# Kernel tuning notes

Hardware: AMD Instinct MI355X
Metric: run time of the kernel (lower is better)

## Reference

```python
import jax, jax.numpy as jnp
import numpy as np

N = 100000
E = 1600000
F = 128
COMP_RATIO = 4
K = max(1, N // COMP_RATIO)


def mean_agg(x, src, tgt, n):
    # mean over in-neighbors: h_i = mean_{(j->i) in edges} x_j
    s = jax.ops.segment_sum(x[src], tgt, num_segments=n)          # [N, F]
    cnt = jax.ops.segment_sum(jnp.ones(src.shape[0], x.dtype), tgt, num_segments=n)
    return s / jnp.maximum(cnt, 1.0)[:, None]


def setup_inputs() -> dict:
    key = jax.random.key(0)
    ks = jax.random.split(key, 10)
    sc = 1.0 / np.sqrt(F)
    return {
        "x": jax.random.normal(ks[0], (N, F), jnp.float32),
        "src": jax.random.randint(ks[1], (E,), 0, N, jnp.int32),
        "tgt": jax.random.randint(ks[2], (E,), 0, N, jnp.int32),
        "W_self": jax.random.normal(ks[3], (F, F), jnp.float32) * sc,
        "W_neigh": jax.random.normal(ks[4], (F, F), jnp.float32) * sc,
        "b_pack": jnp.zeros((F,), jnp.float32),
        "w_score": jax.random.normal(ks[5], (F, 1), jnp.float32) * sc,
        "b_score": jnp.zeros((1,), jnp.float32),
        "W_u1": jax.random.normal(ks[6], (F, F), jnp.float32) * sc,
        "b_u1": jnp.zeros((F,), jnp.float32),
        "W_u2": jax.random.normal(ks[7], (F, F), jnp.float32) * sc,
        "b_u2": jnp.zeros((F,), jnp.float32),
    }


def reference(x, src, tgt, W_self, W_neigh, b_pack, w_score, b_score,
              W_u1, b_u1, W_u2, b_u2):
    # ---- compress ----
    # SAGEConv (mean aggregator): fc_self(x) + fc_neigh(mean_neigh(x)) + bias
    h = x @ W_self + mean_agg(x, src, tgt, N) @ W_neigh + b_pack  # [N, F]
    # scorer: Linear(F,1) + Sigmoid
    score = jax.nn.sigmoid(h @ w_score + b_score)[:, 0]           # [N]
    # pool: topk scores, gate selected features by their score
    sel_scores, idx = jax.lax.top_k(score, K)                     # [K], [K]
    new_val = h[idx] * sel_scores[:, None]                        # [K, F]
    # ---- decompress ----
    z = jnp.zeros((N, F), x.dtype).at[idx].set(new_val)
    # diffusion layer 1 (SageConvExt update_func='diffuse'):
    # propagate neighbor mean, keep the received (seed) features fixed
    d = mean_agg(z, src, tgt, N) @ W_u1 + b_u1
    d = d.at[idx].set(z[idx])
    d = jax.nn.relu(d)
    # diffusion layer 2
    out = mean_agg(d, src, tgt, N) @ W_u2 + b_u2
    out = out.at[idx].set(d[idx])
    return out
```

## Files before the change

### kernel.cpp

```cpp
#include <hip/hip_runtime.h>

#define NN 100000
#define NE 1600000
#define FF 128
#define KK 25000
#define NB ((NN + 255) / 256)
#define BM 64
#define BK 32
#define GEMM_GRID ((NN + BM - 1) / BM)

#define BKT_SHIFT 11
#define NPBK (1 << BKT_SHIFT)
#define NBKT2 ((NN + NPBK - 1) >> BKT_SHIFT)
#define NBLKA 512
#define CHUNKA ((NE + NBLKA - 1) / NBLKA)

__device__ __forceinline__ unsigned short f2b(float f) {
  unsigned u = __float_as_uint(f);
  u += 0x7FFFu + ((u >> 16) & 1u);
  return (unsigned short)(u >> 16);
}
__device__ __forceinline__ unsigned pack2(float lo, float hi) {
  return (unsigned)f2b(lo) | ((unsigned)f2b(hi) << 16);
}

__device__ __forceinline__ unsigned long long topk_key(float s, unsigned i) {
  return (((unsigned long long)__float_as_uint(s)) << 32) |
         (unsigned long long)(0xFFFFFFFFu - i);
}

__global__ __launch_bounds__(256) void k_histA(const int* __restrict__ tgt,
                                               int* __restrict__ histg) {
  __shared__ int h[NBKT2];
  for (int i = threadIdx.x; i < NBKT2; i += 256) h[i] = 0;
  __syncthreads();
  int b = blockIdx.x;
  int e0 = b * CHUNKA, e1 = min(e0 + CHUNKA, NE);
  for (int e = e0 + threadIdx.x; e < e1; e += 256)
    atomicAdd(&h[tgt[e] >> BKT_SHIFT], 1);
  __syncthreads();
  for (int i = threadIdx.x; i < NBKT2; i += 256) histg[i * NBLKA + b] = h[i];
}

__global__ __launch_bounds__(1024) void k_scanA(int* __restrict__ histg,
                                                int* __restrict__ bbase) {
  const int M = NBKT2 * NBLKA;
  const int C = (M + 1023) / 1024;
  __shared__ int part[1024];
  __shared__ int tmp[1024];
  int t = threadIdx.x;
  int i0 = t * C;
  int iend = min(i0 + C, M);
  int s = 0;
  for (int i = i0; i < iend; ++i) s += histg[i];
  part[t] = s;
  __syncthreads();
  int* A = part;
  int* B = tmp;
  for (int off = 1; off < 1024; off <<= 1) {
    int v = A[t] + (t >= off ? A[t - off] : 0);
    B[t] = v;
    __syncthreads();
    int* sw = A; A = B; B = sw;
  }
  int run = (t > 0) ? A[t - 1] : 0;
  for (int i = i0; i < iend; ++i) {
    int v = histg[i];
    histg[i] = run;
    run += v;
  }
  __syncthreads();
  if (t < NBKT2) bbase[t] = histg[t * NBLKA];
  if (t == 0) bbase[NBKT2] = NE;
}

__global__ __launch_bounds__(256) void k_scatterA(const int* __restrict__ src,
                                                  const int* __restrict__ tgt,
                                                  const int* __restrict__ histg,
                                                  int* __restrict__ pairs) {
  __shared__ int cur[NBKT2];
  int b = blockIdx.x;
  for (int i = threadIdx.x; i < NBKT2; i += 256) cur[i] = histg[i * NBLKA + b];
  __syncthreads();
  int e0 = b * CHUNKA, e1 = min(e0 + CHUNKA, NE);
  for (int e = e0 + threadIdx.x; e < e1; e += 256) {
    int t = tgt[e];
    int p = atomicAdd(&cur[t >> BKT_SHIFT], 1);
    pairs[p] = (src[e] << BKT_SHIFT) | (t & (NPBK - 1));
  }
}

__global__ __launch_bounds__(1024) void k_bucketB(const int* __restrict__ pairs,
                                                  const int* __restrict__ bbase,
                                                  int* __restrict__ offsets,
                                                  int* __restrict__ csr) {
  __shared__ int cnt[NPBK];
  __shared__ int part[1024];
  __shared__ int tmp[1024];
  int b = blockIdx.x;
  int t = threadIdx.x;
  int lo = b << BKT_SHIFT;
  int nloc = min(NPBK, NN - lo);
  int base = bbase[b];
  int cntE = bbase[b + 1] - base;
  cnt[t] = 0;
  cnt[t + 1024] = 0;
  __syncthreads();
  for (int p = t; p < cntE; p += 1024)
    atomicAdd(&cnt[pairs[base + p] & (NPBK - 1)], 1);
  __syncthreads();
  int a0 = cnt[2 * t];
  int a1 = cnt[2 * t + 1];
  part[t] = a0 + a1;
  __syncthreads();
  int* A = part;
  int* B = tmp;
  for (int off = 1; off < 1024; off <<= 1) {
    int v = A[t] + (t >= off ? A[t - off] : 0);
    B[t] = v;
    __syncthreads();
    int* sw = A; A = B; B = sw;
  }
  int o0 = (t > 0) ? A[t - 1] : 0;
  int o1 = o0 + a0;
  if (2 * t < nloc) offsets[lo + 2 * t] = base + o0;
  if (2 * t + 1 < nloc) offsets[lo + 2 * t + 1] = base + o1;
  __syncthreads();
  cnt[2 * t] = o0;
  cnt[2 * t + 1] = o1;
  __syncthreads();
  for (int p = t; p < cntE; p += 1024) {
    int v = pairs[base + p];
    int l = v & (NPBK - 1);
    int pos = atomicAdd(&cnt[l], 1);
    csr[base + pos] = v >> BKT_SHIFT;
  }
  if (b == NBKT2 - 1 && t == 0) offsets[NN] = NE;
}

__global__ __launch_bounds__(256) void k_agg(const float* __restrict__ vals,
                                             const int* __restrict__ csr,
                                             const int* __restrict__ offsets,
                                             float* __restrict__ outv) {
  int w = threadIdx.x >> 6;
  int lane = threadIdx.x & 63;
  int half = lane >> 5;
  int li = lane & 31;
  int node = blockIdx.x * 4 + w;
  if (node >= NN) return;
  int beg = offsets[node];
  int end = offsets[node + 1];
  int deg = end - beg;
  float a0 = 0.f, a1 = 0.f, a2 = 0.f, a3 = 0.f;
  int e = beg;
  int e8 = beg + (deg & ~7);
  for (; e < e8; e += 8) {
    float4 v[4];
#pragma unroll
    for (int q = 0; q < 4; ++q) {
      int j = csr[e + 2 * q + half];
      v[q] = *reinterpret_cast<const float4*>(&vals[(size_t)j * FF + li * 4]);
    }
#pragma unroll
    for (int q = 0; q < 4; ++q) {
      a0 += v[q].x; a1 += v[q].y; a2 += v[q].z; a3 += v[q].w;
    }
  }
  for (; e + 2 <= end; e += 2) {
    int j = csr[e + half];
    float4 v = *reinterpret_cast<const float4*>(&vals[(size_t)j * FF + li * 4]);
    a0 += v.x; a1 += v.y; a2 += v.z; a3 += v.w;
  }
  if (e < end && half == 0) {
    int j = csr[e];
    float4 v = *reinterpret_cast<const float4*>(&vals[(size_t)j * FF + li * 4]);
    a0 += v.x; a1 += v.y; a2 += v.z; a3 += v.w;
  }
  a0 += __shfl_xor(a0, 32, 64);
  a1 += __shfl_xor(a1, 32, 64);
  a2 += __shfl_xor(a2, 32, 64);
  a3 += __shfl_xor(a3, 32, 64);
  if (half == 0) {
    float inv = 1.0f / (float)(deg > 0 ? deg : 1);
    *reinterpret_cast<float4*>(&outv[(size_t)node * FF + li * 4]) =
        make_float4(a0 * inv, a1 * inv, a2 * inv, a3 * inv);
  }
}

template <bool GATED>
__global__ __launch_bounds__(256) void k_agg_bf(const unsigned* __restrict__ vals,
                                                const int* __restrict__ csr,
                                                const int* __restrict__ offsets,
                                                const float* __restrict__ sel,
                                                unsigned* __restrict__ outv) {
  int w = threadIdx.x >> 6;
  int lane = threadIdx.x & 63;
  int qt = lane >> 4;
  int li = lane & 15;
  int node = blockIdx.x * 4 + w;
  if (node >= NN) return;
  int beg = offsets[node];
  int end = offsets[node + 1];
  int deg = end - beg;
  float a0 = 0.f, a1 = 0.f, a2 = 0.f, a3 = 0.f;
  float a4 = 0.f, a5 = 0.f, a6 = 0.f, a7 = 0.f;
  int e = beg;
  int e8 = beg + (deg & ~7);
  for (; e < e8; e += 8) {
    uint4 u[2];
#pragma unroll
    for (int q = 0; q < 2; ++q) {
      int j = csr[e + 4 * q + qt];
      u[q] = (!GATED || sel[j] != 0.f)
                 ? *reinterpret_cast<const uint4*>(&vals[(size_t)j * (FF / 2) + li * 4])
                 : make_uint4(0u, 0u, 0u, 0u);
    }
#pragma unroll
    for (int q = 0; q < 2; ++q) {
      a0 += __uint_as_float(u[q].x << 16);
      a1 += __uint_as_float(u[q].x & 0xFFFF0000u);
      a2 += __uint_as_float(u[q].y << 16);
      a3 += __uint_as_float(u[q].y & 0xFFFF0000u);
      a4 += __uint_as_float(u[q].z << 16);
      a5 += __uint_as_float(u[q].z & 0xFFFF0000u);
      a6 += __uint_as_float(u[q].w << 16);
      a7 += __uint_as_float(u[q].w & 0xFFFF0000u);
    }
  }
  for (; e + 4 <= end; e += 4) {
    int j = csr[e + qt];
    uint4 u = (!GATED || sel[j] != 0.f)
                  ? *reinterpret_cast<const uint4*>(&vals[(size_t)j * (FF / 2) + li * 4])
                  : make_uint4(0u, 0u, 0u, 0u);
    a0 += __uint_as_float(u.x << 16);
    a1 += __uint_as_float(u.x & 0xFFFF0000u);
    a2 += __uint_as_float(u.y << 16);
    a3 += __uint_as_float(u.y & 0xFFFF0000u);
    a4 += __uint_as_float(u.z << 16);
    a5 += __uint_as_float(u.z & 0xFFFF0000u);
    a6 += __uint_as_float(u.w << 16);
    a7 += __uint_as_float(u.w & 0xFFFF0000u);
  }
  int r = end - e;
  if (qt < r) {
    int j = csr[e + qt];
    uint4 u = (!GATED || sel[j] != 0.f)
                  ? *reinterpret_cast<const uint4*>(&vals[(size_t)j * (FF / 2) + li * 4])
                  : make_uint4(0u, 0u, 0u, 0u);
    a0 += __uint_as_float(u.x << 16);
    a1 += __uint_as_float(u.x & 0xFFFF0000u);
    a2 += __uint_as_float(u.y << 16);
    a3 += __uint_as_float(u.y & 0xFFFF0000u);
    a4 += __uint_as_float(u.z << 16);
    a5 += __uint_as_float(u.z & 0xFFFF0000u);
    a6 += __uint_as_float(u.w << 16);
    a7 += __uint_as_float(u.w & 0xFFFF0000u);
  }
  a0 += __shfl_xor(a0, 16, 64); a0 += __shfl_xor(a0, 32, 64);
  a1 += __shfl_xor(a1, 16, 64); a1 += __shfl_xor(a1, 32, 64);
  a2 += __shfl_xor(a2, 16, 64); a2 += __shfl_xor(a2, 32, 64);
  a3 += __shfl_xor(a3, 16, 64); a3 += __shfl_xor(a3, 32, 64);
  a4 += __shfl_xor(a4, 16, 64); a4 += __shfl_xor(a4, 32, 64);
  a5 += __shfl_xor(a5, 16, 64); a5 += __shfl_xor(a5, 32, 64);
  a6 += __shfl_xor(a6, 16, 64); a6 += __shfl_xor(a6, 32, 64);
  a7 += __shfl_xor(a7, 16, 64); a7 += __shfl_xor(a7, 32, 64);
  if (qt == 0) {
    float inv = 1.0f / (float)(deg > 0 ? deg : 1);
    uint4 o;
    o.x = pack2(a0 * inv, a1 * inv);
    o.y = pack2(a2 * inv, a3 * inv);
    o.z = pack2(a4 * inv, a5 * inv);
    o.w = pack2(a6 * inv, a7 * inv);
    *reinterpret_cast<uint4*>(&outv[(size_t)node * (FF / 2) + li * 4]) = o;
  }
}

template <int EPI, bool DUAL, bool ABF16>
__global__ __launch_bounds__(256) void k_gemm4(const void* __restrict__ Araw,
                                               const float* __restrict__ W,
                                               const float* __restrict__ A2,
                                               const float* __restrict__ W2,
                                               const float* __restrict__ bias,
                                               const float* __restrict__ aux,
                                               const float* __restrict__ score,
                                               const float* __restrict__ sel,
                                               float* __restrict__ outv,
                                               unsigned* __restrict__ obf,
                                               const float* __restrict__ wsc,
                                               const float* __restrict__ bsc,
                                               float* __restrict__ score_out) {
  __shared__ float As[BK][BM + 4];
  __shared__ float Ws[BK][FF];
  const int tid = threadIdx.x;
  const int tx = tid & 15;
  const int ty = tid >> 4;
  const int m0 = blockIdx.x * BM;

  float acc[4][8];
#pragma unroll
  for (int r = 0; r < 4; ++r)
#pragma unroll
    for (int j = 0; j < 8; ++j) acc[r][j] = 0.f;

  const int NPASS = DUAL ? 2 : 1;
  for (int pass = 0; pass < NPASS; ++pass) {
    const float* Wp = (pass == 0) ? W : W2;
    for (int kt = 0; kt < FF; kt += BK) {
      __syncthreads();
      if (pass == 0 && ABF16) {
        const unsigned* Ab = (const unsigned*)Araw;
#pragma unroll
        for (int t = 0; t < 4; ++t) {
          int i = tid + t * 256;
          int row = i >> 4;
          int cu = i & 15;
          int gr = m0 + row;
          unsigned u = (gr < NN) ? Ab[(size_t)gr * (FF / 2) + (kt >> 1) + cu] : 0u;
          As[cu * 2 + 0][row] = __uint_as_float(u << 16);
          As[cu * 2 + 1][row] = __uint_as_float(u & 0xFFFF0000u);
        }
      } else {
        const float* Ag = (pass == 0) ? (const float*)Araw : A2;
#pragma unroll
        for (int t = 0; t < 2; ++t) {
          int i = tid + t * 256;
          int row = i >> 3;
          int c8 = i & 7;
          int gr = m0 + row;
          float4 v = make_float4(0.f, 0.f, 0.f, 0.f);
          if (gr < NN) v = *(const float4*)&Ag[(size_t)gr * FF + kt + c8 * 4];
          As[c8 * 4 + 0][row] = v.x;
          As[c8 * 4 + 1][row] = v.y;
          As[c8 * 4 + 2][row] = v.z;
          As[c8 * 4 + 3][row] = v.w;
        }
      }
#pragma unroll
      for (int t = 0; t < 4; ++t) {
        int i = tid + t * 256;
        int kr = i >> 5;
        int c4 = i & 31;
        *(float4*)&Ws[kr][c4 * 4] =
            *(const float4*)&Wp[(size_t)(kt + kr) * FF + c4 * 4];
      }
      __syncthreads();
#pragma unroll
      for (int k = 0; k < BK; ++k) {
        float4 a = *(const float4*)&As[k][ty * 4];
        float4 w0 = *(const float4*)&Ws[k][tx * 4];
        float4 w1 = *(const float4*)&Ws[k][tx * 4 + 64];
        float av[4] = {a.x, a.y, a.z, a.w};
        float wv[8] = {w0.x, w0.y, w0.z, w0.w, w1.x, w1.y, w1.z, w1.w};
#pragma unroll
        for (int r = 0; r < 4; ++r)
#pragma unroll
          for (int j = 0; j < 8; ++j) acc[r][j] = fmaf(av[r], wv[j], acc[r][j]);
      }
    }
  }

  float4 b0 = *(const float4*)&bias[tx * 4];
  float4 b1 = *(const float4*)&bias[tx * 4 + 64];
  float bs[8] = {b0.x, b0.y, b0.z, b0.w, b1.x, b1.y, b1.z, b1.w};

  if constexpr (EPI == 0) {
    __shared__ float sp[BM][17];
    float4 s0 = *(const float4*)&wsc[tx * 4];
    float4 s1 = *(const float4*)&wsc[tx * 4 + 64];
    float sv[8] = {s0.x, s0.y, s0.z, s0.w, s1.x, s1.y, s1.z, s1.w};
#pragma unroll
    for (int r = 0; r < 4; ++r) {
      int gi = m0 + ty * 4 + r;
      if (gi >= NN) continue;
      size_t base = (size_t)gi * FF;
      float v[8];
      float p = 0.f;
#pragma unroll
      for (int j = 0; j < 8; ++j) {
        v[j] = acc[r][j] + bs[j];
        p = fmaf(v[j], sv[j], p);
      }
      sp[ty * 4 + r][tx] = p;
      *(float4*)&outv[base + tx * 4] = make_float4(v[0], v[1], v[2], v[3]);
      *(float4*)&outv[base + tx * 4 + 64] = make_float4(v[4], v[5], v[6], v[7]);
    }
    __syncthreads();
    if (tid < BM) {
      int gi = m0 + tid;
      if (gi < NN) {
        float s = 0.f;
#pragma unroll
        for (int t = 0; t < 16; ++t) s += sp[tid][t];
        float z = s + bsc[0];
        score_out[gi] = 1.0f / (1.0f + expf(-z));
      }
    }
  } else {
#pragma unroll
    for (int r = 0; r < 4; ++r) {
      int gi = m0 + ty * 4 + r;
      if (gi >= NN) continue;
      size_t base = (size_t)gi * FF;
      float se = sel[gi];
      if (EPI == 1) {
        float v[8];
        if (se != 0.f) {
          float sc = score[gi];
          float4 x0 = *(const float4*)&aux[base + tx * 4];
          float4 x1 = *(const float4*)&aux[base + tx * 4 + 64];
          float av[8] = {x0.x, x0.y, x0.z, x0.w, x1.x, x1.y, x1.z, x1.w};
#pragma unroll
          for (int j = 0; j < 8; ++j) v[j] = fmaxf(av[j] * sc, 0.f);
          *(float4*)&outv[base + tx * 4] = make_float4(v[0], v[1], v[2], v[3]);
          *(float4*)&outv[base + tx * 4 + 64] = make_float4(v[4], v[5], v[6], v[7]);
        } else {
#pragma unroll
          for (int j = 0; j < 8; ++j) v[j] = fmaxf(acc[r][j] + bs[j], 0.f);
        }
        uint2 p0, p1;
        p0.x = pack2(v[0], v[1]);
        p0.y = pack2(v[2], v[3]);
        p1.x = pack2(v[4], v[5]);
        p1.y = pack2(v[6], v[7]);
        *(uint2*)&obf[(size_t)gi * (FF / 2) + tx * 2] = p0;
        *(uint2*)&obf[(size_t)gi * (FF / 2) + 32 + tx * 2] = p1;
      } else {
        float v[8];
        if (se != 0.f) {
          float4 x0 = *(const float4*)&aux[base + tx * 4];
          float4 x1 = *(const float4*)&aux[base + tx * 4 + 64];
          v[0] = x0.x; v[1] = x0.y; v[2] = x0.z; v[3] = x0.w;
          v[4] = x1.x; v[5] = x1.y; v[6] = x1.z; v[7] = x1.w;
        } else {
#pragma unroll
          for (int j = 0; j < 8; ++j) v[j] = acc[r][j] + bs[j];
        }
        *(float4*)&outv[base + tx * 4] = make_float4(v[0], v[1], v[2], v[3]);
        *(float4*)&outv[base + tx * 4 + 64] = make_float4(v[4], v[5], v[6], v[7]);
      }
    }
  }
}

__global__ void k_init_state(unsigned* state) {
  state[0] = 0u;
  state[1] = 0u;
  state[2] = KK;
}

__global__ __launch_bounds__(256) void k_hist(const float* __restrict__ score,
                                              const unsigned* __restrict__ state,
                                              unsigned* __restrict__ hist,
                                              int bits_fixed) {
  __shared__ unsigned lh[256];
  for (int i = threadIdx.x; i < 256; i += 256) lh[i] = 0;
  __syncthreads();
  unsigned long long prefix =
      (((unsigned long long)state[0]) << 32) | (unsigned long long)state[1];
  int i = blockIdx.x * 256 + threadIdx.x;
  if (i < NN) {
    unsigned long long key = topk_key(score[i], (unsigned)i);
    bool ok = (bits_fixed == 0) ? true : (((key ^ prefix) >> (64 - bits_fixed)) == 0ull);
    if (ok) {
      unsigned b = (unsigned)((key >> (56 - bits_fixed)) & 0xFFull);
      atomicAdd(&lh[b], 1u);
    }
  }
  __syncthreads();
  for (int i2 = threadIdx.x; i2 < 256; i2 += 256)
    if (lh[i2]) atomicAdd(&hist[i2], lh[i2]);
}

__global__ __launch_bounds__(256) void k_select_round(unsigned* __restrict__ state,
                                                      unsigned* __restrict__ hist,
                                                      int bits_fixed) {
  __shared__ unsigned h[256];
  int t = threadIdx.x;
  h[t] = hist[t];
  hist[t] = 0;
  __syncthreads();
  if (t == 0) {
    unsigned rem = state[2];
    unsigned long long prefix =
        (((unsigned long long)state[0]) << 32) | (unsigned long long)state[1];
    unsigned cum = 0;
    int bstar = 0;
    for (int b = 255; b >= 0; --b) {
      unsigned c = h[b];
      if (cum + c >= rem) { bstar = b; break; }
      cum += c;
    }
    rem -= cum;
    prefix |= ((unsigned long long)bstar) << (56 - bits_fixed);
    state[0] = (unsigned)(prefix >> 32);
    state[1] = (unsigned)(prefix & 0xFFFFFFFFull);
    state[2] = rem;
  }
}

__global__ __launch_bounds__(256) void k_gate_zg(const float* __restrict__ h,
                                                 const float* __restrict__ score,
                                                 const unsigned* __restrict__ state,
                                                 float* __restrict__ sel,
                                                 unsigned* __restrict__ zg) {
  int w = threadIdx.x >> 6;
  int lane = threadIdx.x & 63;
  int node = blockIdx.x * 4 + w;
  if (node >= NN) return;
  unsigned long long T =
      (((unsigned long long)state[0]) << 32) | (unsigned long long)state[1];
  float s = score[node];
  bool selected = topk_key(s, (unsigned)node) >= T;
  if (lane == 0) sel[node] = selected ? 1.0f : 0.0f;
  if (!selected) return;
  float2 v = *reinterpret_cast<const float2*>(&h[(size_t)node * FF + lane * 2]);
  zg[(size_t)node * (FF / 2) + lane] = pack2(v.x * s, v.y * s);
}

extern "C" void kernel_launch(void* const* d_in, const int* in_sizes, int n_in,
                              void* d_out, int out_size, void* d_ws, size_t ws_size,
                              hipStream_t stream) {
  const float* x = (const float*)d_in[0];
  const int* src = (const int*)d_in[1];
  const int* tgt = (const int*)d_in[2];
  const float* W_self = (const float*)d_in[3];
  const float* W_neigh = (const float*)d_in[4];
  const float* b_pack = (const float*)d_in[5];
  const float* w_score = (const float*)d_in[6];
  const float* b_score = (const float*)d_in[7];
  const float* W_u1 = (const float*)d_in[8];
  const float* b_u1 = (const float*)d_in[9];
  const float* W_u2 = (const float*)d_in[10];
  const float* b_u2 = (const float*)d_in[11];
  float* out = (float*)d_out;

  char* ws = (char*)d_ws;
  size_t off = 0;
  auto alloc = [&](size_t bytes) -> char* {
    char* p = ws + off;
    off += (bytes + 255) & ~(size_t)255;
    return p;
  };
  int* offsets = (int*)alloc((size_t)(NN + 1) * 4);
  int* csr = (int*)alloc((size_t)NE * 4);
  int* histg = (int*)alloc((size_t)NBKT2 * NBLKA * 4);
  int* bbase = (int*)alloc((size_t)(NBKT2 + 1) * 4);
  float* score = (float*)alloc((size_t)NN * 4);
  float* sel = (float*)alloc((size_t)NN * 4);
  unsigned* hist = (unsigned*)alloc(256 * 4);
  unsigned* state = (unsigned*)alloc(64);
  float* aggF = (float*)alloc((size_t)NN * FF * 4);
  int* pairs = (int*)aggF;
  unsigned* zdbf = (unsigned*)aggF;
  unsigned* aggBF = (unsigned*)(aggF + (size_t)NN * (FF / 2));
  float* bufB = out;

  hipMemsetAsync(hist, 0, 256 * 4, stream);
  k_init_state<<<1, 1, 0, stream>>>(state);

  k_histA<<<NBLKA, 256, 0, stream>>>(tgt, histg);
  k_scanA<<<1, 1024, 0, stream>>>(histg, bbase);
  k_scatterA<<<NBLKA, 256, 0, stream>>>(src, tgt, histg, pairs);
  k_bucketB<<<NBKT2, 1024, 0, stream>>>(pairs, bbase, offsets, csr);

  k_agg<<<NN / 4, 256, 0, stream>>>(x, csr, offsets, aggF);
  k_gemm4<0, true, false><<<GEMM_GRID, 256, 0, stream>>>(
      aggF, W_neigh, x, W_self, b_pack, nullptr, nullptr, nullptr, bufB, nullptr,
      w_score, b_score, score);

  for (int r = 0; r < 8; ++r) {
    k_hist<<<NB, 256, 0, stream>>>(score, state, hist, 8 * r);
    k_select_round<<<1, 256, 0, stream>>>(state, hist, 8 * r);
  }

  k_gate_zg<<<NN / 4, 256, 0, stream>>>(bufB, score, state, sel, zdbf);
  k_agg_bf<true><<<NN / 4, 256, 0, stream>>>(zdbf, csr, offsets, sel, aggBF);
  k_gemm4<1, false, true><<<GEMM_GRID, 256, 0, stream>>>(
      aggBF, W_u1, nullptr, nullptr, b_u1, bufB, score, sel, bufB, zdbf,
      nullptr, nullptr, nullptr);
  k_agg_bf<false><<<NN / 4, 256, 0, stream>>>(zdbf, csr, offsets, nullptr, aggBF);
  k_gemm4<2, false, true><<<GEMM_GRID, 256, 0, stream>>>(
      aggBF, W_u2, nullptr, nullptr, b_u2, bufB, nullptr, sel, out, nullptr,
      nullptr, nullptr, nullptr);
}
```

Measured before the change: 610.5 us.

## Use bf16 MFMA GEMM for diffusion layers with pre-packed weights

Replaces the FP32 SIMT GEMM for the two diffusion-layer linear transforms with a kernel built on the 16x16x32 bf16 MFMA instruction. The bf16 aggregated activations are staged in LDS, and the weights are pre-packed into bf16 MFMA operand layout by a small new kernel. The epilogue now writes outputs per element (scalar stores) rather than as float4 vectors, which may cost some store efficiency. W_u1/W_u2 are rounded to bf16, which reduces precision relative to the FP32 weights used before.

```diff
diff --git a/kernel.cpp b/kernel.cpp
--- a/kernel.cpp
+++ b/kernel.cpp
@@ -14,6 +14,9 @@
 #define NBKT2 ((NN + NPBK - 1) >> BKT_SHIFT)
 #define NBLKA 512
 #define CHUNKA ((NE + NBLKA - 1) / NBLKA)
+
+typedef __attribute__((ext_vector_type(8))) short short8v;
+typedef __attribute__((ext_vector_type(4))) float float4v;
 
 __device__ __forceinline__ unsigned short f2b(float f) {
   unsigned u = __float_as_uint(f);
@@ -395,48 +398,89 @@
         score_out[gi] = 1.0f / (1.0f + expf(-z));
       }
     }
-  } else {
-#pragma unroll
-    for (int r = 0; r < 4; ++r) {
-      int gi = m0 + ty * 4 + r;
+  }
+}
+
+__global__ __launch_bounds__(256) void k_packW(const float* __restrict__ W,
+                                               unsigned* __restrict__ Wpk) {
+  int i = blockIdx.x * 256 + threadIdx.x;
+  int kt = i >> 9;
+  int rem = i & 511;
+  int c = rem >> 2;
+  int h = rem & 3;
+  int kb = kt * 32 + h * 8;
+  uint4 o;
+  o.x = pack2(W[(kb + 0) * FF + c], W[(kb + 1) * FF + c]);
+  o.y = pack2(W[(kb + 2) * FF + c], W[(kb + 3) * FF + c]);
+  o.z = pack2(W[(kb + 4) * FF + c], W[(kb + 5) * FF + c]);
+  o.w = pack2(W[(kb + 6) * FF + c], W[(kb + 7) * FF + c]);
+  *reinterpret_cast<uint4*>(&Wpk[(size_t)i * 4]) = o;
+}
+
+template <int EPI>
+__global__ __launch_bounds__(256) void k_gemm_mfma(const unsigned* __restrict__ A,
+                                                   const unsigned* __restrict__ Wpk,
+                                                   const float* __restrict__ bias,
+                                                   const float* __restrict__ aux,
+                                                   const float* __restrict__ score,
+                                                   const float* __restrict__ sel,
+                                                   float* __restrict__ outv,
+                                                   unsigned short* __restrict__ obf) {
+  __shared__ unsigned As[64][68];
+  const int tid = threadIdx.x;
+  const int wv = tid >> 6;
+  const int l = tid & 63;
+  const int lg = l >> 4;
+  const int lr = l & 15;
+  const int m0 = blockIdx.x * 64;
+
+#pragma unroll
+  for (int p = 0; p < 4; ++p) {
+    int i = tid + p * 256;
+    int row = i >> 4, c4 = (i & 15) * 4;
+    int gr = m0 + row;
+    uint4 v = make_uint4(0u, 0u, 0u, 0u);
+    if (gr < NN) v = *reinterpret_cast<const uint4*>(&A[(size_t)gr * 64 + c4]);
+    *reinterpret_cast<uint4*>(&As[row][c4]) = v;
+  }
+  __syncthreads();
+
+  int arow = wv * 16 + lr;
+  short8v a[4];
+#pragma unroll
+  for (int kt = 0; kt < 4; ++kt)
+    a[kt] = *reinterpret_cast<const short8v*>(&As[arow][kt * 16 + lg * 4]);
+
+#pragma unroll
+  for (int ct = 0; ct < 8; ++ct) {
+    float4v acc = {0.f, 0.f, 0.f, 0.f};
+    int col = ct * 16 + lr;
+#pragma unroll
+    for (int kt = 0; kt < 4; ++kt) {
+      short8v b = *reinterpret_cast<const short8v*>(
+          &Wpk[(size_t)((kt * 128 + col) * 4 + lg) * 4]);
+      acc = __builtin_amdgcn_mfma_f32_16x16x32_bf16(a[kt], b, acc, 0, 0, 0);
+    }
+    float bcol = bias[col];
+#pragma unroll
+    for (int i = 0; i < 4; ++i) {
+      int gi = m0 + wv * 16 + lg * 4 + i;
       if (gi >= NN) continue;
-      size_t base = (size_t)gi * FF;
-      float se = sel[gi];
+      float g = acc[i] + bcol;
+      size_t oi = (size_t)gi * FF + col;
       if (EPI == 1) {
-        float v[8];
+        float se = sel[gi];
+        float v;
         if (se != 0.f) {
-          float sc = score[gi];
-          float4 x0 = *(const float4*)&aux[base + tx * 4];
-          float4 x1 = *(const float4*)&aux[base + tx * 4 + 64];
-          float av[8] = {x0.x, x0.y, x0.z, x0.w, x1.x, x1.y, x1.z, x1.w};
-#pragma unroll
-          for (int j = 0; j < 8; ++j) v[j] = fmaxf(av[j] * sc, 0.f);
-          *(float4*)&outv[base + tx * 4] = make_float4(v[0], v[1], v[2], v[3]);
-          *(float4*)&outv[base + tx * 4 + 64] = make_float4(v[4], v[5], v[6], v[7]);
+          v = fmaxf(aux[oi] * score[gi], 0.f);
+          outv[oi] = v;
         } else {
-#pragma unroll
-          for (int j = 0; j < 8; ++j) v[j] = fmaxf(acc[r][j] + bs[j], 0.f);
+          v = fmaxf(g, 0.f);
         }
-        uint2 p0, p1;
-        p0.x = pack2(v[0], v[1]);
-        p0.y = pack2(v[2], v[3]);
-        p1.x = pack2(v[4], v[5]);
-        p1.y = pack2(v[6], v[7]);
-        *(uint2*)&obf[(size_t)gi * (FF / 2) + tx * 2] = p0;
-        *(uint2*)&obf[(size_t)gi * (FF / 2) + 32 + tx * 2] = p1;
+        obf[(size_t)gi * FF + col] = f2b(v);
       } else {
-        float v[8];
-        if (se != 0.f) {
-          float4 x0 = *(const float4*)&aux[base + tx * 4];
-          float4 x1 = *(const float4*)&aux[base + tx * 4 + 64];
-          v[0] = x0.x; v[1] = x0.y; v[2] = x0.z; v[3] = x0.w;
-          v[4] = x1.x; v[5] = x1.y; v[6] = x1.z; v[7] = x1.w;
-        } else {
-#pragma unroll
-          for (int j = 0; j < 8; ++j) v[j] = acc[r][j] + bs[j];
-        }
-        *(float4*)&outv[base + tx * 4] = make_float4(v[0], v[1], v[2], v[3]);
-        *(float4*)&outv[base + tx * 4 + 64] = make_float4(v[4], v[5], v[6], v[7]);
+        float se = sel[gi];
+        outv[oi] = (se != 0.f) ? aux[oi] : g;
       }
     }
   }
@@ -549,6 +593,8 @@
   float* sel = (float*)alloc((size_t)NN * 4);
   unsigned* hist = (unsigned*)alloc(256 * 4);
   unsigned* state = (unsigned*)alloc(64);
+  unsigned* pkW1 = (unsigned*)alloc(2048 * 16);
+  unsigned* pkW2 = (unsigned*)alloc(2048 * 16);
   float* aggF = (float*)alloc((size_t)NN * FF * 4);
   int* pairs = (int*)aggF;
   unsigned* zdbf = (unsigned*)aggF;
@@ -557,6 +603,8 @@
 
   hipMemsetAsync(hist, 0, 256 * 4, stream);
   k_init_state<<<1, 1, 0, stream>>>(state);
+  k_packW<<<8, 256, 0, stream>>>(W_u1, pkW1);
+  k_packW<<<8, 256, 0, stream>>>(W_u2, pkW2);
 
   k_histA<<<NBLKA, 256, 0, stream>>>(tgt, histg);
   k_scanA<<<1, 1024, 0, stream>>>(histg, bbase);
@@ -575,11 +623,10 @@
 
   k_gate_zg<<<NN / 4, 256, 0, stream>>>(bufB, score, state, sel, zdbf);
   k_agg_bf<true><<<NN / 4, 256, 0, stream>>>(zdbf, csr, offsets, sel, aggBF);
-  k_gemm4<1, false, true><<<GEMM_GRID, 256, 0, stream>>>(
-      aggBF, W_u1, nullptr, nullptr, b_u1, bufB, score, sel, bufB, zdbf,
-      nullptr, nullptr, nullptr);
+  k_gemm_mfma<1><<<GEMM_GRID, 256, 0, stream>>>(aggBF, pkW1, b_u1, bufB, score,
+                                                sel, bufB,
+                                                (unsigned short*)zdbf);
   k_agg_bf<false><<<NN / 4, 256, 0, stream>>>(zdbf, csr, offsets, nullptr, aggBF);
-  k_gemm4<2, false, true><<<GEMM_GRID, 256, 0, stream>>>(
-      aggBF, W_u2, nullptr, nullptr, b_u2, bufB, nullptr, sel, out, nullptr,
-      nullptr, nullptr, nullptr);
-}
+  k_gemm_mfma<2><<<GEMM_GRID, 256, 0, stream>>>(aggBF, pkW2, b_u2, bufB, nullptr,
+                                                sel, out, nullptr);
+}
```

Result: faster. 573.0 us (-6.1%).
